# Kernel tuning notes

Hardware: AMD Instinct MI355X
Metric: run time of the kernel (lower is better)

Reference implementation:

```python
import jax, jax.numpy as jnp
import numpy as np

HIDDEN = 64
GROUPS = 512
GROUP_SIZE = 256  # all groups equal-sized and contiguous in ind_id
N = GROUPS * GROUP_SIZE
NEG_SLOPE = 0.1


def setup_inputs() -> dict:
    key = jax.random.key(0)
    k1, k2, k3 = jax.random.split(key, 3)
    h = jax.random.normal(k1, (N, HIDDEN), dtype=jnp.float32)
    # contiguous equal groups: ind_id = [0,0,...,0,1,1,...]
    ind_id = jnp.repeat(jnp.arange(GROUPS, dtype=jnp.int32), GROUP_SIZE)
    # torch.nn.Linear weights: W.weight [H, H], att.weight [1, 2H+1]
    W = jax.random.normal(k2, (HIDDEN, HIDDEN), dtype=jnp.float32) / np.sqrt(HIDDEN)
    att_w = jax.random.normal(k3, (2 * HIDDEN + 1,), dtype=jnp.float32) / np.sqrt(2 * HIDDEN + 1)
    return {"h": h, "ind_id": ind_id, "W": W, "att_w": att_w}


def reference(h, ind_id, W, att_w):
    # Wh = Linear(h); torch Linear: x @ W.T
    Wh = h @ W.T                                   # [N, H]
    a_src = att_w[:HIDDEN]                         # multiplies Wh_i (row index)
    a_dst = att_w[HIDDEN:2 * HIDDEN]               # multiplies Wh_j (col index)
    a_e = att_w[2 * HIDDEN]                        # multiplies the constant e_ij = 1
    s = Wh @ a_src                                 # [N]
    t = Wh @ a_dst                                 # [N]
    # ind_id is contiguous equal groups -> reshape to [G, M, ...]
    Whg = Wh.reshape(GROUPS, GROUP_SIZE, HIDDEN)
    sg = s.reshape(GROUPS, GROUP_SIZE)
    tg = t.reshape(GROUPS, GROUP_SIZE)
    # e[g,i,j] = leaky_relu(a_src.Wh[i] + a_dst.Wh[j] + a_e)
    e = jax.nn.leaky_relu(sg[:, :, None] + tg[:, None, :] + a_e,
                          negative_slope=NEG_SLOPE)  # [G, M, M]
    alpha = jax.nn.softmax(e, axis=-1)             # softmax over j (torch dim=1)
    out = jnp.einsum('gij,gjh->gih', alpha, Whg)   # [G, M, H]
    return out.reshape(N, HIDDEN)
```

## Files before the change

kernel.cpp:

```cpp
#include <hip/hip_runtime.h>
#include <math.h>

#define NEG_SLOPE 0.1f
#define LOG2E 1.4426950408889634f
#define GROUPS 512

typedef _Float16 half8  __attribute__((ext_vector_type(8)));
typedef _Float16 half4t __attribute__((ext_vector_type(4)));
typedef __fp16   pk16x2 __attribute__((ext_vector_type(2)));
typedef float    f32x4  __attribute__((ext_vector_type(4)));

__device__ __forceinline__ f32x4 mfma_f16(half8 a, half8 b, f32x4 c) {
    return __builtin_amdgcn_mfma_f32_16x16x32_f16(a, b, c, 0, 0, 0);
}

__global__ __launch_bounds__(512, 2)
void egat_fused(const float* __restrict__ Hin,
                const float* __restrict__ Wm,
                const float* __restrict__ att,
                float* __restrict__ Out)
{
    const int g    = blockIdx.x;
    const int tid  = threadIdx.x;
    const int w    = tid >> 6;
    const int lane = tid & 63;
    const int lg   = lane >> 4;
    const int lc   = lane & 15;

    __shared__ __align__(16) _Float16 fragV[8 * 4 * 64 * 8];
    __shared__ __align__(16) _Float16 WtF[2 * 4 * 64 * 8];
    __shared__ __align__(16) float u_lds[128];
    __shared__ __align__(16) float s_lds[256];
    __shared__ __align__(16) float t_lds[256];

    half8 Ahi[2][2], Alo[2][2];
    {
        const float* hbase = Hin + (size_t)(g * 256 + w * 32) * 64;
        #pragma unroll
        for (int it = 0; it < 2; ++it) {
            const float* rp = hbase + (it * 16 + lc) * 64 + lg * 8;
            #pragma unroll
            for (int kt = 0; kt < 2; ++kt) {
                f32x4 f0 = *(const f32x4*)(rp + kt * 32);
                f32x4 f1 = *(const f32x4*)(rp + kt * 32 + 4);
                half8 hi, lo;
                #pragma unroll
                for (int e = 0; e < 4; ++e) {
                    _Float16 a0 = (_Float16)f0[e], a1 = (_Float16)f1[e];
                    hi[e]     = a0;  lo[e]     = (_Float16)(f0[e] - (float)a0);
                    hi[e + 4] = a1;  lo[e + 4] = (_Float16)(f1[e] - (float)a1);
                }
                Ahi[it][kt] = hi;
                Alo[it][kt] = lo;
            }
        }
    }
    const float ae = att[128];

    if (w == 0) {
        float us = 0.f, ut = 0.f;
        #pragma unroll 16
        for (int o = 0; o < 64; ++o) {
            float wv = Wm[o * 64 + lane];
            us = fmaf(wv, att[o], us);
            ut = fmaf(wv, att[64 + o], ut);
        }
        u_lds[lane]      = us;
        u_lds[64 + lane] = ut;
    }

    {
        const int fr = tid;
        const int ln = fr & 63;
        const int ot = (fr >> 6) & 3;
        const int kt = fr >> 8;
        const float* wp = Wm + (ot * 16 + (ln & 15)) * 64 + kt * 32 + (ln >> 4) * 8;
        half8 hi;
        #pragma unroll
        for (int e = 0; e < 8; ++e) hi[e] = (_Float16)wp[e];
        *(half8*)&WtF[fr * 8] = hi;
    }
    __syncthreads();

    half8 Shi[2], Slo[2];
    #pragma unroll
    for (int kt = 0; kt < 2; ++kt) {
        if (lc < 2) {
            const float* up = &u_lds[lc * 64 + kt * 32 + lg * 8];
            f32x4 a = *(const f32x4*)up;
            f32x4 b2 = *(const f32x4*)(up + 4);
            #pragma unroll
            for (int e = 0; e < 4; ++e) {
                _Float16 h0 = (_Float16)a[e], h1 = (_Float16)b2[e];
                Shi[kt][e]     = h0;  Slo[kt][e]     = (_Float16)(a[e] - (float)h0);
                Shi[kt][e + 4] = h1;  Slo[kt][e + 4] = (_Float16)(b2[e] - (float)h1);
            }
        } else {
            #pragma unroll
            for (int e = 0; e < 8; ++e) { Shi[kt][e] = (_Float16)0.f; Slo[kt][e] = (_Float16)0.f; }
        }
    }

    f32x4 acc[2][5];
    #pragma unroll
    for (int it = 0; it < 2; ++it)
        #pragma unroll
        for (int ot = 0; ot < 5; ++ot)
            acc[it][ot] = f32x4{0.f, 0.f, 0.f, 0.f};

    #pragma unroll
    for (int kt = 0; kt < 2; ++kt) {
        #pragma unroll
        for (int ot = 0; ot < 4; ++ot) {
            half8 bh = *(half8*)&WtF[((kt * 4 + ot) * 64 + lane) * 8];
            #pragma unroll
            for (int it = 0; it < 2; ++it)
                acc[it][ot] = mfma_f16(Ahi[it][kt], bh, acc[it][ot]);
        }
        #pragma unroll
        for (int it = 0; it < 2; ++it) {
            acc[it][4] = mfma_f16(Ahi[it][kt], Shi[kt], acc[it][4]);
            acc[it][4] = mfma_f16(Ahi[it][kt], Slo[kt], acc[it][4]);
            acc[it][4] = mfma_f16(Alo[it][kt], Shi[kt], acc[it][4]);
        }
    }

    #pragma unroll
    for (int it = 0; it < 2; ++it) {
        #pragma unroll
        for (int r = 0; r < 4; ++r) {
            int row = w * 32 + it * 16 + lg * 4 + r;
            float v = acc[it][4][r];
            if (lc == 0)      s_lds[row] = (v + ae) * LOG2E;
            else if (lc == 1) t_lds[row] = v * LOG2E;
        }
    }

    #pragma unroll
    for (int it = 0; it < 2; ++it) {
        const int lane2 = (2 * it + (lg >> 1)) * 16 + lc;
        const int eb    = (lg & 1) * 4;
        #pragma unroll
        for (int ot = 0; ot < 4; ++ot) {
            half4t v;
            #pragma unroll
            for (int r = 0; r < 4; ++r) v[r] = (_Float16)acc[it][ot][r];
            *(half4t*)&fragV[((w * 4 + ot) * 64 + lane2) * 8 + eb] = v;
        }
    }
    __syncthreads();

    float sa[2];
    #pragma unroll
    for (int it = 0; it < 2; ++it)
        sa[it] = s_lds[w * 32 + it * 16 + lc];

    half8 ones;
    #pragma unroll
    for (int e = 0; e < 8; ++e) ones[e] = (_Float16)1.f;

    f32x4 acc2[2][5];
    #pragma unroll
    for (int it = 0; it < 2; ++it)
        #pragma unroll
        for (int ot = 0; ot < 5; ++ot)
            acc2[it][ot] = f32x4{0.f, 0.f, 0.f, 0.f};

    for (int ktv = 0; ktv < 8; ++ktv) {
        f32x4 t0 = *(const f32x4*)&t_lds[ktv * 32 + lg * 8];
        f32x4 t1 = *(const f32x4*)&t_lds[ktv * 32 + lg * 8 + 4];
        half8 bfr[4];
        #pragma unroll
        for (int ot = 0; ot < 4; ++ot)
            bfr[ot] = *(half8*)&fragV[((ktv * 4 + ot) * 64 + lane) * 8];

        #pragma unroll
        for (int it = 0; it < 2; ++it) {
            float p[8];
            #pragma unroll
            for (int e = 0; e < 8; ++e) {
                float z = sa[it] + (e < 4 ? t0[e] : t1[e - 4]);
                float x = fmaxf(z, NEG_SLOPE * z);
                p[e] = __builtin_amdgcn_exp2f(x);
            }
            union { pk16x2 h2[4]; half8 h8; } pk;
            #pragma unroll
            for (int e = 0; e < 4; ++e)
                pk.h2[e] = __builtin_amdgcn_cvt_pkrtz(p[2 * e], p[2 * e + 1]);

            acc2[it][4] = mfma_f16(pk.h8, ones, acc2[it][4]);
            #pragma unroll
            for (int ot = 0; ot < 4; ++ot)
                acc2[it][ot] = mfma_f16(pk.h8, bfr[ot], acc2[it][ot]);
        }
    }

    const size_t orow0 = (size_t)(g * 256 + w * 32) * 64;
    #pragma unroll
    for (int it = 0; it < 2; ++it) {
        #pragma unroll
        for (int r = 0; r < 4; ++r) {
            float inv = __builtin_amdgcn_rcpf(acc2[it][4][r]);
            float* op = Out + orow0 + (size_t)(it * 16 + lg * 4 + r) * 64 + lc;
            #pragma unroll
            for (int ot = 0; ot < 4; ++ot)
                op[ot * 16] = acc2[it][ot][r] * inv;
        }
    }
}

extern "C" void kernel_launch(void* const* d_in, const int* in_sizes, int n_in,
                              void* d_out, int out_size, void* d_ws, size_t ws_size,
                              hipStream_t stream) {
    const float* h   = (const float*)d_in[0];
    const float* W   = (const float*)d_in[2];
    const float* att = (const float*)d_in[3];
    float* out = (float*)d_out;
    egat_fused<<<dim3(GROUPS), dim3(512), 0, stream>>>(h, W, att, out);
}
```

Baseline: 24.12 us.

## Split each group across two 256-thread blocks with redundant projection

Launches two blocks per group with 256 threads each. Each block recomputes the full group's Wh projection and s/t scores into LDS, with every wave now handling 64 rows in two passes. Each block then computes attention output for only its half of the query rows. This gives more, smaller blocks for better scheduling and tail balance, at the cost of doing the projection GEMM and reading h twice per group.

New measurement: 30.66 us. +27.1%, slower.

```diff
diff --git a/kernel.cpp b/kernel.cpp
--- a/kernel.cpp
+++ b/kernel.cpp
@@ -14,18 +14,20 @@
     return __builtin_amdgcn_mfma_f32_16x16x32_f16(a, b, c, 0, 0, 0);
 }
 
-__global__ __launch_bounds__(512, 2)
+__global__ __launch_bounds__(256, 2)
 void egat_fused(const float* __restrict__ Hin,
                 const float* __restrict__ Wm,
                 const float* __restrict__ att,
                 float* __restrict__ Out)
 {
-    const int g    = blockIdx.x;
+    const int b    = blockIdx.x;
     const int tid  = threadIdx.x;
     const int w    = tid >> 6;
     const int lane = tid & 63;
     const int lg   = lane >> 4;
     const int lc   = lane & 15;
+    const int g    = b >> 1;
+    const int hb   = b & 1;
 
     __shared__ __align__(16) _Float16 fragV[8 * 4 * 64 * 8];
     __shared__ __align__(16) _Float16 WtF[2 * 4 * 64 * 8];
@@ -33,11 +35,58 @@
     __shared__ __align__(16) float s_lds[256];
     __shared__ __align__(16) float t_lds[256];
 
-    half8 Ahi[2][2], Alo[2][2];
-    {
-        const float* hbase = Hin + (size_t)(g * 256 + w * 32) * 64;
-        #pragma unroll
-        for (int it = 0; it < 2; ++it) {
+    if (w == 0) {
+        float us = 0.f, ut = 0.f;
+        #pragma unroll 16
+        for (int o = 0; o < 64; ++o) {
+            float wv = Wm[o * 64 + lane];
+            us = fmaf(wv, att[o], us);
+            ut = fmaf(wv, att[64 + o], ut);
+        }
+        u_lds[lane]      = us;
+        u_lds[64 + lane] = ut;
+    }
+    #pragma unroll
+    for (int q = 0; q < 2; ++q) {
+        int fr = tid * 2 + q;
+        int ln = fr & 63;
+        int ot = (fr >> 6) & 3;
+        int kt = fr >> 8;
+        const float* wp = Wm + (ot * 16 + (ln & 15)) * 64 + kt * 32 + (ln >> 4) * 8;
+        half8 hi;
+        #pragma unroll
+        for (int e = 0; e < 8; ++e) hi[e] = (_Float16)wp[e];
+        *(half8*)&WtF[fr * 8] = hi;
+    }
+    const float ae = att[128];
+    __syncthreads();
+
+    half8 Shi[2], Slo[2];
+    #pragma unroll
+    for (int kt = 0; kt < 2; ++kt) {
+        if (lc < 2) {
+            const float* up = &u_lds[lc * 64 + kt * 32 + lg * 8];
+            f32x4 a = *(const f32x4*)up;
+            f32x4 b2 = *(const f32x4*)(up + 4);
+            #pragma unroll
+            for (int e = 0; e < 4; ++e) {
+                _Float16 h0 = (_Float16)a[e], h1 = (_Float16)b2[e];
+                Shi[kt][e]     = h0;  Slo[kt][e]     = (_Float16)(a[e] - (float)h0);
+                Shi[kt][e + 4] = h1;  Slo[kt][e + 4] = (_Float16)(b2[e] - (float)h1);
+            }
+        } else {
+            #pragma unroll
+            for (int e = 0; e < 8; ++e) { Shi[kt][e] = (_Float16)0.f; Slo[kt][e] = (_Float16)0.f; }
+        }
+    }
+
+    const float* hbase = Hin + (size_t)(g * 256 + w * 64) * 64;
+    #pragma unroll
+    for (int hp = 0; hp < 2; ++hp) {
+        half8 Ahi[2][2], Alo[2][2];
+        #pragma unroll
+        for (int i = 0; i < 2; ++i) {
+            const int it = hp * 2 + i;
             const float* rp = hbase + (it * 16 + lc) * 64 + lg * 8;
             #pragma unroll
             for (int kt = 0; kt < 2; ++kt) {
@@ -50,110 +99,64 @@
                     hi[e]     = a0;  lo[e]     = (_Float16)(f0[e] - (float)a0);
                     hi[e + 4] = a1;  lo[e + 4] = (_Float16)(f1[e] - (float)a1);
                 }
-                Ahi[it][kt] = hi;
-                Alo[it][kt] = lo;
-            }
-        }
-    }
-    const float ae = att[128];
-
-    if (w == 0) {
-        float us = 0.f, ut = 0.f;
-        #pragma unroll 16
-        for (int o = 0; o < 64; ++o) {
-            float wv = Wm[o * 64 + lane];
-            us = fmaf(wv, att[o], us);
-            ut = fmaf(wv, att[64 + o], ut);
-        }
-        u_lds[lane]      = us;
-        u_lds[64 + lane] = ut;
-    }
-
-    {
-        const int fr = tid;
-        const int ln = fr & 63;
-        const int ot = (fr >> 6) & 3;
-        const int kt = fr >> 8;
-        const float* wp = Wm + (ot * 16 + (ln & 15)) * 64 + kt * 32 + (ln >> 4) * 8;
-        half8 hi;
-        #pragma unroll
-        for (int e = 0; e < 8; ++e) hi[e] = (_Float16)wp[e];
-        *(half8*)&WtF[fr * 8] = hi;
+                Ahi[i][kt] = hi;
+                Alo[i][kt] = lo;
+            }
+        }
+
+        f32x4 acc[2][5];
+        #pragma unroll
+        for (int i = 0; i < 2; ++i)
+            #pragma unroll
+            for (int ot = 0; ot < 5; ++ot)
+                acc[i][ot] = f32x4{0.f, 0.f, 0.f, 0.f};
+
+        #pragma unroll
+        for (int kt = 0; kt < 2; ++kt) {
+            #pragma unroll
+            for (int ot = 0; ot < 4; ++ot) {
+                half8 bh = *(half8*)&WtF[((kt * 4 + ot) * 64 + lane) * 8];
+                #pragma unroll
+                for (int i = 0; i < 2; ++i)
+                    acc[i][ot] = mfma_f16(Ahi[i][kt], bh, acc[i][ot]);
+            }
+            #pragma unroll
+            for (int i = 0; i < 2; ++i) {
+                acc[i][4] = mfma_f16(Ahi[i][kt], Shi[kt], acc[i][4]);
+                acc[i][4] = mfma_f16(Ahi[i][kt], Slo[kt], acc[i][4]);
+                acc[i][4] = mfma_f16(Alo[i][kt], Shi[kt], acc[i][4]);
+            }
+        }
+
+        #pragma unroll
+        for (int i = 0; i < 2; ++i) {
+            const int it = hp * 2 + i;
+            #pragma unroll
+            for (int r = 0; r < 4; ++r) {
+                int row = w * 64 + it * 16 + lg * 4 + r;
+                float v = acc[i][4][r];
+                if (lc == 0)      s_lds[row] = (v + ae) * LOG2E;
+                else if (lc == 1) t_lds[row] = v * LOG2E;
+            }
+            const int ktv   = 2 * w + (it >> 1);
+            const int lane2 = (2 * (it & 1) + (lg >> 1)) * 16 + lc;
+            const int eb    = (lg & 1) * 4;
+            #pragma unroll
+            for (int ot = 0; ot < 4; ++ot) {
+                half4t v;
+                #pragma unroll
+                for (int r = 0; r < 4; ++r) v[r] = (_Float16)acc[i][ot][r];
+                *(half4t*)&fragV[((ktv * 4 + ot) * 64 + lane2) * 8 + eb] = v;
+            }
+        }
     }
     __syncthreads();
 
-    half8 Shi[2], Slo[2];
-    #pragma unroll
-    for (int kt = 0; kt < 2; ++kt) {
-        if (lc < 2) {
-            const float* up = &u_lds[lc * 64 + kt * 32 + lg * 8];
-            f32x4 a = *(const f32x4*)up;
-            f32x4 b2 = *(const f32x4*)(up + 4);
-            #pragma unroll
-            for (int e = 0; e < 4; ++e) {
-                _Float16 h0 = (_Float16)a[e], h1 = (_Float16)b2[e];
-                Shi[kt][e]     = h0;  Slo[kt][e]     = (_Float16)(a[e] - (float)h0);
-                Shi[kt][e + 4] = h1;  Slo[kt][e + 4] = (_Float16)(b2[e] - (float)h1);
-            }
-        } else {
-            #pragma unroll
-            for (int e = 0; e < 8; ++e) { Shi[kt][e] = (_Float16)0.f; Slo[kt][e] = (_Float16)0.f; }
-        }
-    }
-
-    f32x4 acc[2][5];
+    const int rbase = hb * 128 + w * 32;
+    float sa[2];
     #pragma unroll
     for (int it = 0; it < 2; ++it)
-        #pragma unroll
-        for (int ot = 0; ot < 5; ++ot)
-            acc[it][ot] = f32x4{0.f, 0.f, 0.f, 0.f};
-
-    #pragma unroll
-    for (int kt = 0; kt < 2; ++kt) {
-        #pragma unroll
-        for (int ot = 0; ot < 4; ++ot) {
-            half8 bh = *(half8*)&WtF[((kt * 4 + ot) * 64 + lane) * 8];
-            #pragma unroll
-            for (int it = 0; it < 2; ++it)
-                acc[it][ot] = mfma_f16(Ahi[it][kt], bh, acc[it][ot]);
-        }
-        #pragma unroll
-        for (int it = 0; it < 2; ++it) {
-            acc[it][4] = mfma_f16(Ahi[it][kt], Shi[kt], acc[it][4]);
-            acc[it][4] = mfma_f16(Ahi[it][kt], Slo[kt], acc[it][4]);
-            acc[it][4] = mfma_f16(Alo[it][kt], Shi[kt], acc[it][4]);
-        }
-    }
-
-    #pragma unroll
-    for (int it = 0; it < 2; ++it) {
-        #pragma unroll
-        for (int r = 0; r < 4; ++r) {
-            int row = w * 32 + it * 16 + lg * 4 + r;
-            float v = acc[it][4][r];
-            if (lc == 0)      s_lds[row] = (v + ae) * LOG2E;
-            else if (lc == 1) t_lds[row] = v * LOG2E;
-        }
-    }
-
-    #pragma unroll
-    for (int it = 0; it < 2; ++it) {
-        const int lane2 = (2 * it + (lg >> 1)) * 16 + lc;
-        const int eb    = (lg & 1) * 4;
-        #pragma unroll
-        for (int ot = 0; ot < 4; ++ot) {
-            half4t v;
-            #pragma unroll
-            for (int r = 0; r < 4; ++r) v[r] = (_Float16)acc[it][ot][r];
-            *(half4t*)&fragV[((w * 4 + ot) * 64 + lane2) * 8 + eb] = v;
-        }
-    }
-    __syncthreads();
-
-    float sa[2];
-    #pragma unroll
-    for (int it = 0; it < 2; ++it)
-        sa[it] = s_lds[w * 32 + it * 16 + lc];
+        sa[it] = s_lds[rbase + it * 16 + lc];
 
     half8 ones;
     #pragma unroll
@@ -176,17 +179,17 @@
 
         #pragma unroll
         for (int it = 0; it < 2; ++it) {
-            float p[8];
+            float pr[8];
             #pragma unroll
             for (int e = 0; e < 8; ++e) {
                 float z = sa[it] + (e < 4 ? t0[e] : t1[e - 4]);
                 float x = fmaxf(z, NEG_SLOPE * z);
-                p[e] = __builtin_amdgcn_exp2f(x);
+                pr[e] = __builtin_amdgcn_exp2f(x);
             }
             union { pk16x2 h2[4]; half8 h8; } pk;
             #pragma unroll
             for (int e = 0; e < 4; ++e)
-                pk.h2[e] = __builtin_amdgcn_cvt_pkrtz(p[2 * e], p[2 * e + 1]);
+                pk.h2[e] = __builtin_amdgcn_cvt_pkrtz(pr[2 * e], pr[2 * e + 1]);
 
             acc2[it][4] = mfma_f16(pk.h8, ones, acc2[it][4]);
             #pragma unroll
@@ -195,7 +198,7 @@
         }
     }
 
-    const size_t orow0 = (size_t)(g * 256 + w * 32) * 64;
+    const size_t orow0 = (size_t)(g * 256 + rbase) * 64;
     #pragma unroll
     for (int it = 0; it < 2; ++it) {
         #pragma unroll
@@ -216,5 +219,5 @@
     const float* W   = (const float*)d_in[2];
     const float* att = (const float*)d_in[3];
     float* out = (float*)d_out;
-    egat_fused<<<dim3(GROUPS), dim3(512), 0, stream>>>(h, W, att, out);
+    egat_fused<<<dim3(2 * GROUPS), dim3(256), 0, stream>>>(h, W, att, out);
 }
```

## Precompute fp16 weight fragments in a prep kernel shared by all blocks

Applied to the files above, without the earlier changes.

Adds a single-block prep kernel that computes the attention projection vectors (W^T·a, pre-scaled by log2e) and writes the fp16 MFMA fragments of W and the hi/lo split projection fragments to workspace. The main kernel then loads these fragments directly from global memory. This removes the per-block W conversion, the serial projection loop in wave 0, one __syncthreads and some LDS. It costs an extra kernel launch with a serial dependency, and the fragments are now read from global/L2 instead of LDS.

Result: slower. 27.00 us (+11.9%).

```diff
diff --git a/kernel.cpp b/kernel.cpp
--- a/kernel.cpp
+++ b/kernel.cpp
@@ -14,9 +14,61 @@
     return __builtin_amdgcn_mfma_f32_16x16x32_f16(a, b, c, 0, 0, 0);
 }
 
+
+__global__ void egat_wprep(const float* __restrict__ Wm,
+                           const float* __restrict__ att,
+                           _Float16* __restrict__ wtf,
+                           _Float16* __restrict__ wst)
+{
+    __shared__ float u[128];
+    const int tid = threadIdx.x;
+
+    if (tid < 128) {
+        const int which = tid >> 6;
+        const int k     = tid & 63;
+        float s = 0.f;
+        #pragma unroll 16
+        for (int o = 0; o < 64; ++o)
+            s = fmaf(Wm[o * 64 + k], att[which * 64 + o], s);
+        u[tid] = s * LOG2E;
+    }
+    __syncthreads();
+
+    #pragma unroll
+    for (int q = 0; q < 2; ++q) {
+        int fr = tid * 2 + q;
+        int ln = fr & 63;
+        int ot = (fr >> 6) & 3;
+        int kt = fr >> 8;
+        const float* wp = Wm + (ot * 16 + (ln & 15)) * 64 + kt * 32 + (ln >> 4) * 8;
+        half8 hi;
+        #pragma unroll
+        for (int e = 0; e < 8; ++e) hi[e] = (_Float16)wp[e];
+        *(half8*)&wtf[fr * 8] = hi;
+    }
+
+    if (tid < 128) {
+        const int kt  = tid >> 6;
+        const int ln  = tid & 63;
+        const int col = ln & 15;
+        const int k0  = kt * 32 + (ln >> 4) * 8;
+        half8 hi, lo;
+        #pragma unroll
+        for (int e = 0; e < 8; ++e) {
+            float v = (col == 0) ? u[k0 + e] : (col == 1 ? u[64 + k0 + e] : 0.f);
+            _Float16 h0 = (_Float16)v;
+            hi[e] = h0;
+            lo[e] = (_Float16)(v - (float)h0);
+        }
+        *(half8*)&wst[(kt * 64 + ln) * 8]       = hi;
+        *(half8*)&wst[((2 + kt) * 64 + ln) * 8] = lo;
+    }
+}
+
 __global__ __launch_bounds__(512, 2)
 void egat_fused(const float* __restrict__ Hin,
-                const float* __restrict__ Wm,
+                const _Float16* __restrict__ wtf,
+                const _Float16* __restrict__ wst,
                 const float* __restrict__ att,
                 float* __restrict__ Out)
 {
@@ -28,8 +80,6 @@
     const int lc   = lane & 15;
 
     __shared__ __align__(16) _Float16 fragV[8 * 4 * 64 * 8];
-    __shared__ __align__(16) _Float16 WtF[2 * 4 * 64 * 8];
-    __shared__ __align__(16) float u_lds[128];
     __shared__ __align__(16) float s_lds[256];
     __shared__ __align__(16) float t_lds[256];
 
@@ -55,51 +105,13 @@
             }
         }
     }
-    const float ae = att[128];
-
-    if (w == 0) {
-        float us = 0.f, ut = 0.f;
-        #pragma unroll 16
-        for (int o = 0; o < 64; ++o) {
-            float wv = Wm[o * 64 + lane];
-            us = fmaf(wv, att[o], us);
-            ut = fmaf(wv, att[64 + o], ut);
-        }
-        u_lds[lane]      = us;
-        u_lds[64 + lane] = ut;
-    }
-
-    {
-        const int fr = tid;
-        const int ln = fr & 63;
-        const int ot = (fr >> 6) & 3;
-        const int kt = fr >> 8;
-        const float* wp = Wm + (ot * 16 + (ln & 15)) * 64 + kt * 32 + (ln >> 4) * 8;
-        half8 hi;
-        #pragma unroll
-        for (int e = 0; e < 8; ++e) hi[e] = (_Float16)wp[e];
-        *(half8*)&WtF[fr * 8] = hi;
-    }
-    __syncthreads();
-
     half8 Shi[2], Slo[2];
     #pragma unroll
     for (int kt = 0; kt < 2; ++kt) {
-        if (lc < 2) {
-            const float* up = &u_lds[lc * 64 + kt * 32 + lg * 8];
-            f32x4 a = *(const f32x4*)up;
-            f32x4 b2 = *(const f32x4*)(up + 4);
-            #pragma unroll
-            for (int e = 0; e < 4; ++e) {
-                _Float16 h0 = (_Float16)a[e], h1 = (_Float16)b2[e];
-                Shi[kt][e]     = h0;  Slo[kt][e]     = (_Float16)(a[e] - (float)h0);
-                Shi[kt][e + 4] = h1;  Slo[kt][e + 4] = (_Float16)(b2[e] - (float)h1);
-            }
-        } else {
-            #pragma unroll
-            for (int e = 0; e < 8; ++e) { Shi[kt][e] = (_Float16)0.f; Slo[kt][e] = (_Float16)0.f; }
-        }
-    }
+        Shi[kt] = *(const half8*)&wst[(kt * 64 + lane) * 8];
+        Slo[kt] = *(const half8*)&wst[((2 + kt) * 64 + lane) * 8];
+    }
+    const float aeL = att[128] * LOG2E;
 
     f32x4 acc[2][5];
     #pragma unroll
@@ -112,7 +124,7 @@
     for (int kt = 0; kt < 2; ++kt) {
         #pragma unroll
         for (int ot = 0; ot < 4; ++ot) {
-            half8 bh = *(half8*)&WtF[((kt * 4 + ot) * 64 + lane) * 8];
+            half8 bh = *(const half8*)&wtf[((kt * 4 + ot) * 64 + lane) * 8];
             #pragma unroll
             for (int it = 0; it < 2; ++it)
                 acc[it][ot] = mfma_f16(Ahi[it][kt], bh, acc[it][ot]);
@@ -131,8 +143,8 @@
         for (int r = 0; r < 4; ++r) {
             int row = w * 32 + it * 16 + lg * 4 + r;
             float v = acc[it][4][r];
-            if (lc == 0)      s_lds[row] = (v + ae) * LOG2E;
-            else if (lc == 1) t_lds[row] = v * LOG2E;
+            if (lc == 0)      s_lds[row] = v + aeL;
+            else if (lc == 1) t_lds[row] = v;
         }
     }
 
@@ -216,5 +228,10 @@
     const float* W   = (const float*)d_in[2];
     const float* att = (const float*)d_in[3];
     float* out = (float*)d_out;
-    egat_fused<<<dim3(GROUPS), dim3(512), 0, stream>>>(h, W, att, out);
-}
+
+    _Float16* wtf = (_Float16*)d_ws;
+    _Float16* wst = (_Float16*)d_ws + 4096;
+
+    egat_wprep<<<dim3(1),      dim3(256), 0, stream>>>(W, att, wtf, wst);
+    egat_fused<<<dim3(GROUPS), dim3(512), 0, stream>>>(h, wtf, wst, att, out);
+}
```
